# Performance work log

Measured on AMD Instinct MI355X. Metric: run time of the kernel, lower is better.

Reference implementation:

```python
import jax, jax.numpy as jnp
import numpy as np
from jax import lax

EPS = 1e-5
NUM_GROUPS = 32
OFFSET_SCALE = 1.0
K = 3            # deformable conv kernel size
KK = K * K
DWK = 7          # depthwise kernel size for offset predictor


def group_norm(x, gamma, beta, num_groups=NUM_GROUPS):
    B, C, H, W = x.shape
    xg = x.reshape(B, num_groups, C // num_groups, H, W)
    m = xg.mean(axis=(2, 3, 4), keepdims=True)
    v = xg.var(axis=(2, 3, 4), keepdims=True)
    xn = ((xg - m) * lax.rsqrt(v + EPS)).reshape(B, C, H, W)
    return xn * gamma[None, :, None, None] + beta[None, :, None, None]


def bilinear_gather(x, py, px):
    # x: [B,C,H,W]; py, px: [B,KK,H,W] absolute sample coords -> [B,C,KK,H,W]
    B, C, H, W = x.shape
    y0 = jnp.floor(py)
    x0 = jnp.floor(px)
    wy1 = py - y0
    wx1 = px - x0
    wy0 = 1.0 - wy1
    wx0 = 1.0 - wx1
    xf = x.reshape(B, C, H * W)

    def gather(yi, xi):
        valid = (yi >= 0) & (yi <= H - 1) & (xi >= 0) & (xi <= W - 1)
        yc = jnp.clip(yi, 0, H - 1).astype(jnp.int32)
        xc = jnp.clip(xi, 0, W - 1).astype(jnp.int32)
        idx = (yc * W + xc).reshape(B, -1)                      # [B, KK*H*W]
        g = jax.vmap(lambda a, i: a[:, i])(xf, idx)             # [B, C, KK*H*W]
        g = g.reshape(B, C, KK, H, W)
        return g * valid.astype(x.dtype)[:, None]

    out = (gather(y0, x0) * (wy0 * wx0)[:, None]
           + gather(y0, x0 + 1.0) * (wy0 * wx1)[:, None]
           + gather(y0 + 1.0, x0) * (wy1 * wx0)[:, None]
           + gather(y0 + 1.0, x0 + 1.0) * (wy1 * wx1)[:, None])
    return out


def deform_conv(x, dw, pw, pwb, w, b):
    # x: [B,C,H,W]; dw: [C,1,DWK,DWK] depthwise; pw: [2*KK,C,1,1]; w: [O,C,K,K]
    B, C, H, W = x.shape
    dn = ('NCHW', 'OIHW', 'NCHW')
    f = lax.conv_general_dilated(x, dw, (1, 1), 'SAME',
                                 feature_group_count=C, dimension_numbers=dn)
    off = lax.conv_general_dilated(f, pw, (1, 1), 'SAME', dimension_numbers=dn)
    off = (off + pwb[None, :, None, None]) * OFFSET_SCALE       # [B,2*KK,H,W]
    off = off.reshape(B, KK, 2, H, W)
    ks = jnp.arange(K, dtype=x.dtype) - (K - 1) / 2             # [-1,0,1]
    ky = jnp.repeat(ks, K)                                      # [KK]
    kx = jnp.tile(ks, K)
    yy, xx = jnp.meshgrid(jnp.arange(H, dtype=x.dtype),
                          jnp.arange(W, dtype=x.dtype), indexing='ij')
    py = yy[None, None] + ky[None, :, None, None] + off[:, :, 0]  # [B,KK,H,W]
    px = xx[None, None] + kx[None, :, None, None] + off[:, :, 1]
    sampled = bilinear_gather(x, py, px)                        # [B,C,KK,H,W]
    O = w.shape[0]
    out = jnp.einsum('bckhw,ock->bohw', sampled, w.reshape(O, C, KK))
    return out + b[None, :, None, None]


def setup_inputs() -> dict:
    key = jax.random.key(0)
    ks = jax.random.split(key, 10)
    B, C, H, W = 4, 256, 64, 64
    O = C
    x = jax.random.normal(ks[0], (B, C, H, W), dtype=jnp.float32)

    def conv_w(k, shape, fan_in):
        return jax.random.normal(k, shape, dtype=jnp.float32) / np.sqrt(fan_in)

    inp = {
        'x': x,
        'gn1_g': jnp.ones((C,), jnp.float32), 'gn1_b': jnp.zeros((C,), jnp.float32),
        'dw1': conv_w(ks[1], (C, 1, DWK, DWK), DWK * DWK),
        'pw1': jax.random.normal(ks[2], (2 * KK, C, 1, 1), jnp.float32) * 0.01,
        'pwb1': jnp.zeros((2 * KK,), jnp.float32),
        'w1': conv_w(ks[3], (O, C, K, K), C * KK),
        'b1': jnp.zeros((O,), jnp.float32),
        'gn2_g': jnp.ones((O,), jnp.float32), 'gn2_b': jnp.zeros((O,), jnp.float32),
        'dw2': conv_w(ks[4], (O, 1, DWK, DWK), DWK * DWK),
        'pw2': jax.random.normal(ks[5], (2 * KK, O, 1, 1), jnp.float32) * 0.01,
        'pwb2': jnp.zeros((2 * KK,), jnp.float32),
        'w2': conv_w(ks[6], (O, O, K, K), O * KK),
        'b2': jnp.zeros((O,), jnp.float32),
    }
    return inp


def reference(x, gn1_g, gn1_b, dw1, pw1, pwb1, w1, b1,
              gn2_g, gn2_b, dw2, pw2, pwb2, w2, b2):
    h = jax.nn.relu(group_norm(x, gn1_g, gn1_b))
    h = deform_conv(h, dw1, pw1, pwb1, w1, b1)
    h = jax.nn.relu(group_norm(h, gn2_g, gn2_b))
    # Dropout / DropPath are identity in eval mode
    h = deform_conv(h, dw2, pw2, pwb2, w2, b2)
    return h + x  # shortcut is Identity (in_channels == out_channels)
```

## Files before the change

kernel.cpp:

```cpp
#include <hip/hip_runtime.h>

#define B_    4
#define C_    256
#define H_    64
#define W_    64
#define HW_   4096
#define NG_   32
#define CPG_  8
#define KK_   9
#define NOFF_ 18

typedef __attribute__((ext_vector_type(8))) short short8;
typedef __attribute__((ext_vector_type(4))) short short4v;
typedef __attribute__((ext_vector_type(4))) float floatx4;

static __device__ __forceinline__ short f2bf(float f) {
    union { float f; unsigned u; } v; v.f = f;
    unsigned r = v.u + 0x7fff + ((v.u >> 16) & 1);
    return (short)(r >> 16);
}
static __device__ __forceinline__ float bf2f(short s) {
    union { unsigned u; float f; } v;
    v.u = ((unsigned)(unsigned short)s) << 16;
    return v.f;
}

__global__ __launch_bounds__(256) void prep_kernel(
    const float* __restrict__ w1, const float* __restrict__ w2,
    const float* __restrict__ pw1, const float* __restrict__ pw2,
    const float* __restrict__ x,
    short* __restrict__ wp1, short* __restrict__ wp2,
    short* __restrict__ ppk1, short* __restrict__ ppk2,
    float2* __restrict__ stats1, float* __restrict__ gsum,
    float* __restrict__ gss)
{
    int blk = blockIdx.x;
    int t = threadIdx.x;
    if (blk < 4608) {
        const float* w = (blk < 2304) ? w1 : w2;
        short* wp = (blk < 2304) ? wp1 : wp2;
        int idx = (blk % 2304) * 256 + t;
        int j    = idx & 7;
        int lane = (idx >> 3) & 63;
        int ot   = (idx >> 9) & 15;
        int slab = idx >> 13;
        int k = slab >> 3, cc = slab & 7;
        int o = ot * 16 + (lane & 15);
        int c = cc * 32 + (lane >> 4) * 8 + j;
        wp[idx] = f2bf(w[(size_t)(o * C_ + c) * KK_ + k]);
    } else if (blk < 4672) {
        int q = blk - 4608;
        const float* pw = (q < 32) ? pw1 : pw2;
        short* ppk = (q < 32) ? ppk1 : ppk2;
        int idx = (q & 31) * 256 + t;
        int j = idx & 7, lane = (idx >> 3) & 63;
        int ot = (idx >> 9) & 1, sl = idx >> 10;
        int o = ot * 16 + (lane & 15);
        int k = sl * 32 + (lane >> 4) * 8 + j;
        ppk[idx] = (o < NOFF_) ? f2bf(pw[o * C_ + k]) : (short)0;
    } else if (blk < 4800) {
        int q = blk - 4672;
        size_t base = (size_t)q * CPG_ * HW_;
        const float4* in4 = (const float4*)(x + base);
        float s = 0.f, ss = 0.f;
        for (int i = t; i < 8192; i += 256) {
            float4 v = in4[i];
            s  += v.x + v.y + v.z + v.w;
            ss += v.x * v.x + v.y * v.y + v.z * v.z + v.w * v.w;
        }
        #pragma unroll
        for (int d = 32; d > 0; d >>= 1) {
            s  += __shfl_down(s, d, 64);
            ss += __shfl_down(ss, d, 64);
        }
        __shared__ float red[8];
        int wid = t >> 6;
        if ((t & 63) == 0) { red[wid] = s; red[4 + wid] = ss; }
        __syncthreads();
        if (t == 0) {
            float S  = red[0] + red[1] + red[2] + red[3];
            float SS = red[4] + red[5] + red[6] + red[7];
            float m = S / 32768.f;
            float var = SS / 32768.f - m * m;
            stats1[q] = make_float2(m, rsqrtf(var + 1e-5f));
        }
    } else {
        if (t < 128) { gsum[t] = 0.f; gss[t] = 0.f; }
    }
}

__global__ __launch_bounds__(256) void gnt_kernel(
    const float* __restrict__ xin, const short* __restrict__ yin,
    const float2* __restrict__ stats1, const float* __restrict__ gsum,
    const float* __restrict__ gss, const float* __restrict__ gamma,
    const float* __restrict__ beta, short* __restrict__ hbf,
    short* __restrict__ hbt, int layer)
{
    int q = blockIdx.x;
    int b = q >> 6;
    int px0 = (q & 63) * 64;
    __shared__ unsigned ltile[64 * 132];
    __shared__ float2 sst[32];
    int t = threadIdx.x;
    if (t < 32) {
        float m, rs;
        if (layer == 1) { float2 v = stats1[b * 32 + t]; m = v.x; rs = v.y; }
        else {
            float s = gsum[b * 32 + t], ss = gss[b * 32 + t];
            m = s / 32768.f;
            float var = ss / 32768.f - m * m;
            rs = rsqrtf(var + 1e-5f);
        }
        sst[t] = make_float2(m, rs);
    }
    __syncthreads();
    int pq4 = t & 15, cphi = t >> 4;
    #pragma unroll
    for (int i = 0; i < 8; ++i) {
        int cp = i * 16 + cphi;
        int c0 = 2 * cp, c1 = c0 + 1;
        float2 st = sst[c0 >> 3];
        float ga0 = gamma[c0] * st.y, be0 = beta[c0] - st.x * ga0;
        float ga1 = gamma[c1] * st.y, be1 = beta[c1] - st.x * ga1;
        short4v lo, hi;
        if (layer == 1) {
            const float* r0 = xin + (size_t)(b * C_ + c0) * HW_ + px0 + pq4 * 4;
            float4 v0 = *(const float4*)r0;
            float4 v1 = *(const float4*)(r0 + HW_);
            lo.x = f2bf(fmaxf(fmaf(v0.x, ga0, be0), 0.f));
            lo.y = f2bf(fmaxf(fmaf(v0.y, ga0, be0), 0.f));
            lo.z = f2bf(fmaxf(fmaf(v0.z, ga0, be0), 0.f));
            lo.w = f2bf(fmaxf(fmaf(v0.w, ga0, be0), 0.f));
            hi.x = f2bf(fmaxf(fmaf(v1.x, ga1, be1), 0.f));
            hi.y = f2bf(fmaxf(fmaf(v1.y, ga1, be1), 0.f));
            hi.z = f2bf(fmaxf(fmaf(v1.z, ga1, be1), 0.f));
            hi.w = f2bf(fmaxf(fmaf(v1.w, ga1, be1), 0.f));
        } else {
            const short* r0 = yin + (size_t)(b * C_ + c0) * HW_ + px0 + pq4 * 4;
            short4v v0 = *(const short4v*)r0;
            short4v v1 = *(const short4v*)(r0 + HW_);
            lo.x = f2bf(fmaxf(fmaf(bf2f(v0.x), ga0, be0), 0.f));
            lo.y = f2bf(fmaxf(fmaf(bf2f(v0.y), ga0, be0), 0.f));
            lo.z = f2bf(fmaxf(fmaf(bf2f(v0.z), ga0, be0), 0.f));
            lo.w = f2bf(fmaxf(fmaf(bf2f(v0.w), ga0, be0), 0.f));
            hi.x = f2bf(fmaxf(fmaf(bf2f(v1.x), ga1, be1), 0.f));
            hi.y = f2bf(fmaxf(fmaf(bf2f(v1.y), ga1, be1), 0.f));
            hi.z = f2bf(fmaxf(fmaf(bf2f(v1.z), ga1, be1), 0.f));
            hi.w = f2bf(fmaxf(fmaf(bf2f(v1.w), ga1, be1), 0.f));
        }
        *(short4v*)(hbf + (size_t)(b * C_ + c0) * HW_ + px0 + pq4 * 4) = lo;
        *(short4v*)(hbf + (size_t)(b * C_ + c1) * HW_ + px0 + pq4 * 4) = hi;
        #pragma unroll
        for (int j = 0; j < 4; ++j) {
            int pl = pq4 * 4 + j;
            unsigned wrd = (unsigned)(unsigned short)lo[j]
                         | ((unsigned)(unsigned short)hi[j] << 16);
            ltile[pl * 132 + (cp ^ ((pl & 7) << 2))] = wrd;
        }
    }
    __syncthreads();
    int co = t & 31, ph = t >> 5;
    #pragma unroll
    for (int r = 0; r < 8; ++r) {
        int pl = r * 8 + ph;
        uint4 v = *(const uint4*)&ltile[pl * 132 + ((co * 4) ^ ((pl & 7) << 2))];
        *(uint4*)(hbt + ((size_t)b * HW_ + px0 + pl) * C_ + co * 8) = v;
    }
}

__global__ __launch_bounds__(256) void dw7_kernel(
    const short* __restrict__ in, const float* __restrict__ dwk,
    short* __restrict__ out)
{
    int plane = blockIdx.x;
    int c = plane & (C_ - 1);
    const short* src = in + (size_t)plane * HW_;
    short* dst = out + (size_t)plane * HW_;
    __shared__ float tile[70 * 72];
    __shared__ float wk[49];
    int t = threadIdx.x;
    if (t < 49) wk[t] = dwk[c * 49 + t];
    for (int i = t; i < 70 * 72; i += 256) tile[i] = 0.f;
    __syncthreads();
    const short4v* src4 = (const short4v*)src;
    for (int i = t; i < HW_ / 4; i += 256) {
        short4v v = src4[i];
        int y = i >> 4, x = (i & 15) * 4;
        float* tp = &tile[(y + 3) * 72 + (x + 3)];
        tp[0] = bf2f(v.x); tp[1] = bf2f(v.y);
        tp[2] = bf2f(v.z); tp[3] = bf2f(v.w);
    }
    __syncthreads();
    #pragma unroll
    for (int it = 0; it < 4; ++it) {
        int idx = it * 256 + t;
        int y = idx >> 4;
        int x0 = (idx & 15) * 4;
        float a0 = 0.f, a1 = 0.f, a2 = 0.f, a3 = 0.f;
        #pragma unroll
        for (int dy = 0; dy < 7; ++dy) {
            const float* tr = &tile[(y + dy) * 72 + x0];
            float4 ra = *(const float4*)tr;
            float4 rb = *(const float4*)(tr + 4);
            float4 rc = *(const float4*)(tr + 8);
            float r[12] = {ra.x, ra.y, ra.z, ra.w,
                           rb.x, rb.y, rb.z, rb.w,
                           rc.x, rc.y, rc.z, rc.w};
            const float* wr = &wk[dy * 7];
            #pragma unroll
            for (int dx = 0; dx < 7; ++dx) {
                float wv = wr[dx];
                a0 = fmaf(r[dx], wv, a0);
                a1 = fmaf(r[dx + 1], wv, a1);
                a2 = fmaf(r[dx + 2], wv, a2);
                a3 = fmaf(r[dx + 3], wv, a3);
            }
        }
        short4v o;
        o.x = f2bf(a0); o.y = f2bf(a1); o.z = f2bf(a2); o.w = f2bf(a3);
        *(short4v*)&dst[y * 64 + x0] = o;
    }
}

__global__ __launch_bounds__(1024, 4) void deform_fused_kernel(
    const short* __restrict__ hbt,  const short* __restrict__ fdwc,
    const short* __restrict__ ppk,  const float* __restrict__ pwb,
    const short* __restrict__ wp,   const float* __restrict__ bias,
    const float* __restrict__ resid, float* __restrict__ outf,
    short* __restrict__ outb, float* __restrict__ gsum,
    float* __restrict__ gss)
{
    int b = blockIdx.x >> 6;
    int row = blockIdx.x & 63;
    __shared__ __align__(16) short sbuf[2][16384];
    __shared__ int   pidx[576];
    __shared__ float cf[576][4];
    __shared__ float off_lds[NOFF_ * 64];
    int t = threadIdx.x;
    int wv = t >> 6, lane = t & 63;
    int pq = lane >> 4, pr = lane & 15;

    short* ftile = &sbuf[0][0];
    {
        int c = t >> 2, seg = t & 3;
        const short* src = fdwc + (size_t)(b * C_ + c) * HW_ + row * 64;
        *(short8*)&ftile[c * 64 + seg * 8]       = *(const short8*)(src + seg * 8);
        *(short8*)&ftile[c * 64 + (seg + 4) * 8] = *(const short8*)(src + (seg + 4) * 8);
    }
    __syncthreads();

    if (wv < 8) {
        int ot = wv & 1, ptw = wv >> 1;
        int pxl = ptw * 16 + pr;
        const short8* ap = (const short8*)ppk;
        floatx4 pacc = (floatx4){0.f, 0.f, 0.f, 0.f};
        #pragma unroll
        for (int sl = 0; sl < 8; ++sl) {
            short8 bf;
            int cbase = sl * 32 + pq * 8;
            #pragma unroll
            for (int j = 0; j < 8; ++j) bf[j] = ftile[(cbase + j) * 64 + pxl];
            short8 af = ap[(sl * 2 + ot) * 64 + lane];
            pacc = __builtin_amdgcn_mfma_f32_16x16x32_bf16(af, bf, pacc, 0, 0, 0);
        }
        #pragma unroll
        for (int r = 0; r < 4; ++r) {
            int o = ot * 16 + pq * 4 + r;
            if (o < NOFF_) off_lds[o * 64 + pxl] = pacc[r] + pwb[o];
        }
    }
    __syncthreads();

    if (t < 576) {
        int k = t >> 6, p = t & 63;
        float offy = off_lds[(2 * k) * 64 + p];
        float offx = off_lds[(2 * k + 1) * 64 + p];
        float py = (float)row + (float)(k / 3 - 1) + offy;
        float px = (float)p   + (float)(k % 3 - 1) + offx;
        float y0f = floorf(py), x0f = floorf(px);
        float wy1 = py - y0f, wx1 = px - x0f;
        float wy0 = 1.f - wy1, wx0 = 1.f - wx1;
        float y1f = y0f + 1.f, x1f = x0f + 1.f;
        bool vy0 = (y0f >= 0.f) && (y0f <= 63.f);
        bool vy1 = (y1f >= 0.f) && (y1f <= 63.f);
        bool vx0 = (x0f >= 0.f) && (x0f <= 63.f);
        bool vx1 = (x1f >= 0.f) && (x1f <= 63.f);
        int iy0 = (int)fminf(fmaxf(y0f, 0.f), 63.f);
        int iy1 = (int)fminf(fmaxf(y1f, 0.f), 63.f);
        int ix0 = (int)fminf(fmaxf(x0f, 0.f), 63.f);
        int ix1 = (int)fminf(fmaxf(x1f, 0.f), 63.f);
        pidx[t] = iy0 | (ix0 << 8) | (iy1 << 16) | (ix1 << 24);
        cf[t][0] = (vy0 && vx0) ? wy0 * wx0 : 0.f;
        cf[t][1] = (vy0 && vx1) ? wy0 * wx1 : 0.f;
        cf[t][2] = (vy1 && vx0) ? wy1 * wx0 : 0.f;
        cf[t][3] = (vy1 && vx1) ? wy1 * wx1 : 0.f;
    }
    __syncthreads();

    int ssl0 = t >> 8;
    int spx = (t >> 2) & 63, scb = t & 3;
    int u2 = spx * 4 + (scb ^ ((spx + (spx >> 2)) & 3));
    const short* hb0 = hbt + ((size_t)b * HW_) * C_ + ssl0 * 32 + scb * 8;
    const short* hb1 = hb0 + 128;

    short8 rs0[8], rs1[8];
    auto prefetch = [&](int g, short8* r) {
        int pk = pidx[g * 64 + spx];
        int iy0 = pk & 255, ix0 = (pk >> 8) & 255;
        int iy1 = (pk >> 16) & 255, ix1 = (pk >> 24) & 255;
        size_t a00 = (size_t)(iy0 * 64 + ix0) * C_;
        size_t a01 = (size_t)(iy0 * 64 + ix1) * C_;
        size_t a10 = (size_t)(iy1 * 64 + ix0) * C_;
        size_t a11 = (size_t)(iy1 * 64 + ix1) * C_;
        r[0] = *(const short8*)(hb0 + a00);
        r[1] = *(const short8*)(hb0 + a01);
        r[2] = *(const short8*)(hb0 + a10);
        r[3] = *(const short8*)(hb0 + a11);
        r[4] = *(const short8*)(hb1 + a00);
        r[5] = *(const short8*)(hb1 + a01);
        r[6] = *(const short8*)(hb1 + a10);
        r[7] = *(const short8*)(hb1 + a11);
    };
    auto stage_write = [&](int g, int bi, const short8* r) {
        int e = g * 64 + spx;
        float w00 = cf[e][0], w01 = cf[e][1], w10 = cf[e][2], w11 = cf[e][3];
        short8 va, vb;
        #pragma unroll
        for (int j = 0; j < 8; ++j) {
            va[j] = f2bf(w00 * bf2f(r[0][j]) + w01 * bf2f(r[1][j])
                       + w10 * bf2f(r[2][j]) + w11 * bf2f(r[3][j]));
            vb[j] = f2bf(w00 * bf2f(r[4][j]) + w01 * bf2f(r[5][j])
                       + w10 * bf2f(r[6][j]) + w11 * bf2f(r[7][j]));
        }
        *(short8*)&sbuf[bi][ssl0 * 2048 + u2 * 8] = va;
        *(short8*)&sbuf[bi][(ssl0 + 4) * 2048 + u2 * 8] = vb;
    };

    floatx4 acc[4];
    #pragma unroll
    for (int pt = 0; pt < 4; ++pt) acc[pt] = (floatx4){0.f, 0.f, 0.f, 0.f};
    int ub[4];
    #pragma unroll
    for (int pt = 0; pt < 4; ++pt) {
        int px2 = pt * 16 + pr;
        ub[pt] = px2 * 4 + (pq ^ ((px2 + (px2 >> 2)) & 3));
    }

    prefetch(0, rs0);
    stage_write(0, 0, rs0);
    prefetch(1, rs1);
    __syncthreads();

    const short8* wp8 = (const short8*)wp;
    #pragma unroll
    for (int g = 0; g < 9; ++g) {
        if (g + 2 < 9) prefetch(g + 2, (g & 1) ? rs1 : rs0);
        const short* sb = sbuf[g & 1];
        #pragma unroll
        for (int half = 0; half < 2; ++half) {
            short8 af[4];
            #pragma unroll
            for (int q2 = 0; q2 < 4; ++q2)
                af[q2] = wp8[(size_t)((g * 8 + half * 4 + q2) * 16 + wv) * 64 + lane];
            #pragma unroll
            for (int q2 = 0; q2 < 4; ++q2) {
                int s2 = half * 4 + q2;
                #pragma unroll
                for (int pt = 0; pt < 4; ++pt) {
                    short8 bfv = *(const short8*)&sb[s2 * 2048 + ub[pt] * 8];
                    acc[pt] = __builtin_amdgcn_mfma_f32_16x16x32_bf16(
                        af[q2], bfv, acc[pt], 0, 0, 0);
                }
            }
        }
        if (g + 1 < 9)
            stage_write(g + 1, (g + 1) & 1, (g & 1) ? rs0 : rs1);
        __syncthreads();
    }

    float ssum = 0.f, ssq = 0.f;
    #pragma unroll
    for (int r = 0; r < 4; ++r) {
        int o = wv * 16 + pq * 4 + r;
        float bo = bias[o];
        size_t obase = ((size_t)(b * C_ + o)) * HW_ + row * 64 + pr;
        #pragma unroll
        for (int pt = 0; pt < 4; ++pt) {
            float v = acc[pt][r] + bo;
            if (outf) {
                outf[obase + pt * 16] = v + resid[obase + pt * 16];
            } else {
                short sv = f2bf(v);
                outb[obase + pt * 16] = sv;
                float vq = bf2f(sv);
                ssum += vq; ssq += vq * vq;
            }
        }
    }
    if (outb) {
        #pragma unroll
        for (int d = 1; d < 32; d <<= 1) {
            ssum += __shfl_xor(ssum, d, 64);
            ssq  += __shfl_xor(ssq, d, 64);
        }
        if ((lane & 31) == 0) {
            int grp = wv * 2 + (pq >> 1);
            atomicAdd(&gsum[b * 32 + grp], ssum);
            atomicAdd(&gss[b * 32 + grp], ssq);
        }
    }
}

extern "C" void kernel_launch(void* const* d_in, const int* in_sizes, int n_in,
                              void* d_out, int out_size, void* d_ws, size_t ws_size,
                              hipStream_t stream)
{
    const float* x     = (const float*)d_in[0];
    const float* gn1_g = (const float*)d_in[1];
    const float* gn1_b = (const float*)d_in[2];
    const float* dw1   = (const float*)d_in[3];
    const float* pw1   = (const float*)d_in[4];
    const float* pwb1  = (const float*)d_in[5];
    const float* w1    = (const float*)d_in[6];
    const float* b1    = (const float*)d_in[7];
    const float* gn2_g = (const float*)d_in[8];
    const float* gn2_b = (const float*)d_in[9];
    const float* dw2   = (const float*)d_in[10];
    const float* pw2   = (const float*)d_in[11];
    const float* pwb2  = (const float*)d_in[12];
    const float* w2    = (const float*)d_in[13];
    const float* b2    = (const float*)d_in[14];
    float* out = (float*)d_out;

    float* ws   = (float*)d_ws;
    short* y1b    = (short*)ws;
    short* hbf    = (short*)(ws + 2097152);
    short* hbt    = (short*)(ws + 4194304);
    short* fdwc   = (short*)(ws + 6291456);
    short* wp1    = (short*)(ws + 8388608);
    short* wp2    = (short*)(ws + 8683520);
    short* ppk1   = (short*)(ws + 8978432);
    short* ppk2   = (short*)(ws + 8982528);
    float2* st1   = (float2*)(ws + 8986624);
    float* gsum   = ws + 8986880;
    float* gss    = ws + 8987008;

    prep_kernel<<<4801, 256, 0, stream>>>(w1, w2, pw1, pw2, x,
                                          wp1, wp2, ppk1, ppk2,
                                          st1, gsum, gss);

    gnt_kernel<<<256, 256, 0, stream>>>(x, nullptr, st1, gsum, gss,
                                        gn1_g, gn1_b, hbf, hbt, 1);
    dw7_kernel<<<B_ * C_, 256, 0, stream>>>(hbf, dw1, fdwc);
    deform_fused_kernel<<<B_ * H_, 1024, 0, stream>>>(
        hbt, fdwc, ppk1, pwb1, wp1, b1, nullptr, nullptr, y1b, gsum, gss);

    gnt_kernel<<<256, 256, 0, stream>>>(nullptr, y1b, st1, gsum, gss,
                                        gn2_g, gn2_b, hbf, hbt, 2);
    dw7_kernel<<<B_ * C_, 256, 0, stream>>>(hbf, dw2, fdwc);
    deform_fused_kernel<<<B_ * H_, 1024, 0, stream>>>(
        hbt, fdwc, ppk2, pwb2, wp2, b2, x, out, nullptr, nullptr, nullptr);
}
```

Baseline: 263.6 us.

## Fuse all stages into one cooperative persistent kernel with grid syncs

```diff
diff --git a/kernel.cpp b/kernel.cpp
--- a/kernel.cpp
+++ b/kernel.cpp
@@ -1,4 +1,7 @@
 #include <hip/hip_runtime.h>
+#include <hip/hip_cooperative_groups.h>
+
+namespace cg = cooperative_groups;
 
 #define B_    4
 #define C_    256
@@ -25,99 +28,31 @@
     return v.f;
 }
 
-__global__ __launch_bounds__(256) void prep_kernel(
-    const float* __restrict__ w1, const float* __restrict__ w2,
-    const float* __restrict__ pw1, const float* __restrict__ pw2,
-    const float* __restrict__ x,
-    short* __restrict__ wp1, short* __restrict__ wp2,
-    short* __restrict__ ppk1, short* __restrict__ ppk2,
-    float2* __restrict__ stats1, float* __restrict__ gsum,
-    float* __restrict__ gss)
+static __device__ __forceinline__ void gnt_phase(
+    char* smem, int layer, const float* xin, const short* yin,
+    const float2* st1, const float* gsum, const float* gss,
+    const float* gamma, const float* beta, short* hbt)
 {
-    int blk = blockIdx.x;
-    int t = threadIdx.x;
-    if (blk < 4608) {
-        const float* w = (blk < 2304) ? w1 : w2;
-        short* wp = (blk < 2304) ? wp1 : wp2;
-        int idx = (blk % 2304) * 256 + t;
-        int j    = idx & 7;
-        int lane = (idx >> 3) & 63;
-        int ot   = (idx >> 9) & 15;
-        int slab = idx >> 13;
-        int k = slab >> 3, cc = slab & 7;
-        int o = ot * 16 + (lane & 15);
-        int c = cc * 32 + (lane >> 4) * 8 + j;
-        wp[idx] = f2bf(w[(size_t)(o * C_ + c) * KK_ + k]);
-    } else if (blk < 4672) {
-        int q = blk - 4608;
-        const float* pw = (q < 32) ? pw1 : pw2;
-        short* ppk = (q < 32) ? ppk1 : ppk2;
-        int idx = (q & 31) * 256 + t;
-        int j = idx & 7, lane = (idx >> 3) & 63;
-        int ot = (idx >> 9) & 1, sl = idx >> 10;
-        int o = ot * 16 + (lane & 15);
-        int k = sl * 32 + (lane >> 4) * 8 + j;
-        ppk[idx] = (o < NOFF_) ? f2bf(pw[o * C_ + k]) : (short)0;
-    } else if (blk < 4800) {
-        int q = blk - 4672;
-        size_t base = (size_t)q * CPG_ * HW_;
-        const float4* in4 = (const float4*)(x + base);
-        float s = 0.f, ss = 0.f;
-        for (int i = t; i < 8192; i += 256) {
-            float4 v = in4[i];
-            s  += v.x + v.y + v.z + v.w;
-            ss += v.x * v.x + v.y * v.y + v.z * v.z + v.w * v.w;
-        }
-        #pragma unroll
-        for (int d = 32; d > 0; d >>= 1) {
-            s  += __shfl_down(s, d, 64);
-            ss += __shfl_down(ss, d, 64);
-        }
-        __shared__ float red[8];
-        int wid = t >> 6;
-        if ((t & 63) == 0) { red[wid] = s; red[4 + wid] = ss; }
-        __syncthreads();
-        if (t == 0) {
-            float S  = red[0] + red[1] + red[2] + red[3];
-            float SS = red[4] + red[5] + red[6] + red[7];
-            float m = S / 32768.f;
-            float var = SS / 32768.f - m * m;
-            stats1[q] = make_float2(m, rsqrtf(var + 1e-5f));
-        }
-    } else {
-        if (t < 128) { gsum[t] = 0.f; gss[t] = 0.f; }
-    }
-}
-
-__global__ __launch_bounds__(256) void gnt_kernel(
-    const float* __restrict__ xin, const short* __restrict__ yin,
-    const float2* __restrict__ stats1, const float* __restrict__ gsum,
-    const float* __restrict__ gss, const float* __restrict__ gamma,
-    const float* __restrict__ beta, short* __restrict__ hbf,
-    short* __restrict__ hbt, int layer)
-{
-    int q = blockIdx.x;
-    int b = q >> 6;
-    int px0 = (q & 63) * 64;
-    __shared__ unsigned ltile[64 * 132];
-    __shared__ float2 sst[32];
-    int t = threadIdx.x;
+    unsigned* ltile = (unsigned*)smem;
+    float2* sst = (float2*)(smem + 33792);
+    int blk = blockIdx.x, t = threadIdx.x;
+    int b = blk >> 6;
+    int px0 = (blk & 63) * 64;
     if (t < 32) {
         float m, rs;
-        if (layer == 1) { float2 v = stats1[b * 32 + t]; m = v.x; rs = v.y; }
+        if (layer == 1) { float2 v = st1[b * 32 + t]; m = v.x; rs = v.y; }
         else {
             float s = gsum[b * 32 + t], ss = gss[b * 32 + t];
             m = s / 32768.f;
-            float var = ss / 32768.f - m * m;
-            rs = rsqrtf(var + 1e-5f);
+            rs = rsqrtf(ss / 32768.f - m * m + 1e-5f);
         }
         sst[t] = make_float2(m, rs);
     }
     __syncthreads();
     int pq4 = t & 15, cphi = t >> 4;
     #pragma unroll
-    for (int i = 0; i < 8; ++i) {
-        int cp = i * 16 + cphi;
+    for (int i = 0; i < 2; ++i) {
+        int cp = i * 64 + cphi;
         int c0 = 2 * cp, c1 = c0 + 1;
         float2 st = sst[c0 >> 3];
         float ga0 = gamma[c0] * st.y, be0 = beta[c0] - st.x * ga0;
@@ -148,8 +83,6 @@
             hi.z = f2bf(fmaxf(fmaf(bf2f(v1.z), ga1, be1), 0.f));
             hi.w = f2bf(fmaxf(fmaf(bf2f(v1.w), ga1, be1), 0.f));
         }
-        *(short4v*)(hbf + (size_t)(b * C_ + c0) * HW_ + px0 + pq4 * 4) = lo;
-        *(short4v*)(hbf + (size_t)(b * C_ + c1) * HW_ + px0 + pq4 * 4) = hi;
         #pragma unroll
         for (int j = 0; j < 4; ++j) {
             int pl = pq4 * 4 + j;
@@ -161,39 +94,64 @@
     __syncthreads();
     int co = t & 31, ph = t >> 5;
     #pragma unroll
-    for (int r = 0; r < 8; ++r) {
-        int pl = r * 8 + ph;
+    for (int r = 0; r < 2; ++r) {
+        int pl = r * 32 + ph;
         uint4 v = *(const uint4*)&ltile[pl * 132 + ((co * 4) ^ ((pl & 7) << 2))];
         *(uint4*)(hbt + ((size_t)b * HW_ + px0 + pl) * C_ + co * 8) = v;
     }
 }
 
-__global__ __launch_bounds__(256) void dw7_kernel(
-    const short* __restrict__ in, const float* __restrict__ dwk,
-    short* __restrict__ out)
+static __device__ __forceinline__ void dw7_phase(
+    char* smem, int layer, const float* xin, const short* yin,
+    const float2* st1, const float* gsum, const float* gss,
+    const float* gamma, const float* beta, const float* dwk,
+    short* fdwc)
 {
-    int plane = blockIdx.x;
-    int c = plane & (C_ - 1);
-    const short* src = in + (size_t)plane * HW_;
-    short* dst = out + (size_t)plane * HW_;
-    __shared__ float tile[70 * 72];
-    __shared__ float wk[49];
     int t = threadIdx.x;
-    if (t < 49) wk[t] = dwk[c * 49 + t];
-    for (int i = t; i < 70 * 72; i += 256) tile[i] = 0.f;
-    __syncthreads();
-    const short4v* src4 = (const short4v*)src;
-    for (int i = t; i < HW_ / 4; i += 256) {
-        short4v v = src4[i];
-        int y = i >> 4, x = (i & 15) * 4;
-        float* tp = &tile[(y + 3) * 72 + (x + 3)];
-        tp[0] = bf2f(v.x); tp[1] = bf2f(v.y);
-        tp[2] = bf2f(v.z); tp[3] = bf2f(v.w);
-    }
-    __syncthreads();
+    int q = t >> 8, tq = t & 255;
+    int plane = blockIdx.x * 4 + q;
+    int b = plane >> 8, c = plane & (C_ - 1);
+    float* tile = (float*)(smem + q * 20480);
+    float* wk = tile + 5040;
+    float m, rs;
+    if (layer == 1) { float2 s = st1[b * 32 + (c >> 3)]; m = s.x; rs = s.y; }
+    else {
+        float s = gsum[b * 32 + (c >> 3)], ss = gss[b * 32 + (c >> 3)];
+        m = s / 32768.f;
+        rs = rsqrtf(ss / 32768.f - m * m + 1e-5f);
+    }
+    float ga = gamma[c] * rs, be = beta[c] - m * ga;
+    if (tq < 49) wk[tq] = dwk[c * 49 + tq];
+    for (int i = tq; i < 5040; i += 256) tile[i] = 0.f;
+    __syncthreads();
+    if (layer == 1) {
+        const float4* src4 = (const float4*)(xin + (size_t)plane * HW_);
+        for (int i = tq; i < 1024; i += 256) {
+            float4 v = src4[i];
+            int y = i >> 4, xx = (i & 15) * 4;
+            float* tp = &tile[(y + 3) * 72 + xx + 3];
+            tp[0] = fmaxf(fmaf(v.x, ga, be), 0.f);
+            tp[1] = fmaxf(fmaf(v.y, ga, be), 0.f);
+            tp[2] = fmaxf(fmaf(v.z, ga, be), 0.f);
+            tp[3] = fmaxf(fmaf(v.w, ga, be), 0.f);
+        }
+    } else {
+        const short4v* src4 = (const short4v*)(yin + (size_t)plane * HW_);
+        for (int i = tq; i < 1024; i += 256) {
+            short4v v = src4[i];
+            int y = i >> 4, xx = (i & 15) * 4;
+            float* tp = &tile[(y + 3) * 72 + xx + 3];
+            tp[0] = fmaxf(fmaf(bf2f(v.x), ga, be), 0.f);
+            tp[1] = fmaxf(fmaf(bf2f(v.y), ga, be), 0.f);
+            tp[2] = fmaxf(fmaf(bf2f(v.z), ga, be), 0.f);
+            tp[3] = fmaxf(fmaf(bf2f(v.w), ga, be), 0.f);
+        }
+    }
+    __syncthreads();
+    short* dst = fdwc + (size_t)plane * HW_;
     #pragma unroll
     for (int it = 0; it < 4; ++it) {
-        int idx = it * 256 + t;
+        int idx = it * 256 + tq;
         int y = idx >> 4;
         int x0 = (idx & 15) * 4;
         float a0 = 0.f, a1 = 0.f, a2 = 0.f, a3 = 0.f;
@@ -222,30 +180,28 @@
     }
 }
 
-__global__ __launch_bounds__(1024, 4) void deform_fused_kernel(
-    const short* __restrict__ hbt,  const short* __restrict__ fdwc,
-    const short* __restrict__ ppk,  const float* __restrict__ pwb,
-    const short* __restrict__ wp,   const float* __restrict__ bias,
-    const float* __restrict__ resid, float* __restrict__ outf,
-    short* __restrict__ outb, float* __restrict__ gsum,
-    float* __restrict__ gss)
+static __device__ __forceinline__ void deform_phase(
+    char* smem, const short* hbt, const short* fdwc, const short* ppk,
+    const float* pwb, const short* wp, const float* bias,
+    const float* resid, float* outf, short* outb,
+    float* gsum, float* gss)
 {
+    short* sbufA = (short*)smem;
+    short* sbufB = (short*)(smem + 32768);
+    int*   pidx  = (int*)(smem + 65536);
+    float (*cf)[4] = (float(*)[4])(smem + 67840);
+    float* off_lds = (float*)(smem + 77056);
     int b = blockIdx.x >> 6;
     int row = blockIdx.x & 63;
-    __shared__ __align__(16) short sbuf[2][16384];
-    __shared__ int   pidx[576];
-    __shared__ float cf[576][4];
-    __shared__ float off_lds[NOFF_ * 64];
     int t = threadIdx.x;
     int wv = t >> 6, lane = t & 63;
     int pq = lane >> 4, pr = lane & 15;
 
-    short* ftile = &sbuf[0][0];
     {
         int c = t >> 2, seg = t & 3;
         const short* src = fdwc + (size_t)(b * C_ + c) * HW_ + row * 64;
-        *(short8*)&ftile[c * 64 + seg * 8]       = *(const short8*)(src + seg * 8);
-        *(short8*)&ftile[c * 64 + (seg + 4) * 8] = *(const short8*)(src + (seg + 4) * 8);
+        *(short8*)&sbufA[c * 64 + seg * 8]       = *(const short8*)(src + seg * 8);
+        *(short8*)&sbufA[c * 64 + (seg + 4) * 8] = *(const short8*)(src + (seg + 4) * 8);
     }
     __syncthreads();
 
@@ -259,7 +215,7 @@
             short8 bf;
             int cbase = sl * 32 + pq * 8;
             #pragma unroll
-            for (int j = 0; j < 8; ++j) bf[j] = ftile[(cbase + j) * 64 + pxl];
+            for (int j = 0; j < 8; ++j) bf[j] = sbufA[(cbase + j) * 64 + pxl];
             short8 af = ap[(sl * 2 + ot) * 64 + lane];
             pacc = __builtin_amdgcn_mfma_f32_16x16x32_bf16(af, bf, pacc, 0, 0, 0);
         }
@@ -332,8 +288,9 @@
             vb[j] = f2bf(w00 * bf2f(r[4][j]) + w01 * bf2f(r[5][j])
                        + w10 * bf2f(r[6][j]) + w11 * bf2f(r[7][j]));
         }
-        *(short8*)&sbuf[bi][ssl0 * 2048 + u2 * 8] = va;
-        *(short8*)&sbuf[bi][(ssl0 + 4) * 2048 + u2 * 8] = vb;
+        short* sb = bi ? sbufB : sbufA;
+        *(short8*)&sb[ssl0 * 2048 + u2 * 8] = va;
+        *(short8*)&sb[(ssl0 + 4) * 2048 + u2 * 8] = vb;
     };
 
     floatx4 acc[4];
@@ -352,10 +309,8 @@
     __syncthreads();
 
     const short8* wp8 = (const short8*)wp;
-    #pragma unroll
     for (int g = 0; g < 9; ++g) {
-        if (g + 2 < 9) prefetch(g + 2, (g & 1) ? rs1 : rs0);
-        const short* sb = sbuf[g & 1];
+        const short* sb = (g & 1) ? sbufB : sbufA;
         #pragma unroll
         for (int half = 0; half < 2; ++half) {
             short8 af[4];
@@ -373,8 +328,10 @@
                 }
             }
         }
-        if (g + 1 < 9)
+        if (g + 1 < 9) {
             stage_write(g + 1, (g + 1) & 1, (g & 1) ? rs0 : rs1);
+            if (g + 2 < 9) prefetch(g + 2, (g & 1) ? rs1 : rs0);
+        }
         __syncthreads();
     }
 
@@ -409,6 +366,106 @@
             atomicAdd(&gss[b * 32 + grp], ssq);
         }
     }
+}
+
+__global__ __launch_bounds__(1024) void mono_kernel(
+    const float* __restrict__ x,
+    const float* __restrict__ gn1_g, const float* __restrict__ gn1_b,
+    const float* __restrict__ dw1, const float* __restrict__ pw1,
+    const float* __restrict__ pwb1, const float* __restrict__ w1,
+    const float* __restrict__ b1,
+    const float* __restrict__ gn2_g, const float* __restrict__ gn2_b,
+    const float* __restrict__ dw2, const float* __restrict__ pw2,
+    const float* __restrict__ pwb2, const float* __restrict__ w2,
+    const float* __restrict__ b2,
+    float* __restrict__ out,
+    short* __restrict__ hbt1, short* __restrict__ fdwc1,
+    short* __restrict__ hbt2, short* __restrict__ fdwc2,
+    short* __restrict__ y1b,
+    short* __restrict__ wp1, short* __restrict__ wp2,
+    short* __restrict__ ppk1, short* __restrict__ ppk2,
+    float2* __restrict__ st1, float* __restrict__ gsum,
+    float* __restrict__ gss)
+{
+    cg::grid_group grid = cg::this_grid();
+    __shared__ __align__(16) char smem[81920];
+    int blk = blockIdx.x, t = threadIdx.x;
+
+    if (blk < 128) {
+        size_t base = (size_t)blk * CPG_ * HW_;
+        const float4* in4 = (const float4*)(x + base);
+        float s = 0.f, ss = 0.f;
+        for (int i = t; i < 8192; i += 1024) {
+            float4 v = in4[i];
+            s  += v.x + v.y + v.z + v.w;
+            ss += v.x * v.x + v.y * v.y + v.z * v.z + v.w * v.w;
+        }
+        #pragma unroll
+        for (int d = 32; d > 0; d >>= 1) {
+            s  += __shfl_down(s, d, 64);
+            ss += __shfl_down(ss, d, 64);
+        }
+        float* red = (float*)smem;
+        int wid = t >> 6;
+        if ((t & 63) == 0) { red[wid] = s; red[16 + wid] = ss; }
+        __syncthreads();
+        if (t == 0) {
+            float S = 0.f, SS = 0.f;
+            #pragma unroll
+            for (int i = 0; i < 16; ++i) { S += red[i]; SS += red[16 + i]; }
+            float m = S / 32768.f;
+            float var = SS / 32768.f - m * m;
+            st1[blk] = make_float2(m, rsqrtf(var + 1e-5f));
+        }
+    } else {
+        int tid = (blk - 128) * 1024 + t;
+        for (int idx = tid; idx < 589824; idx += 131072) {
+            int j    = idx & 7;
+            int lane = (idx >> 3) & 63;
+            int ot   = (idx >> 9) & 15;
+            int slab = idx >> 13;
+            int k = slab >> 3, cc = slab & 7;
+            int o = ot * 16 + (lane & 15);
+            int c = cc * 32 + (lane >> 4) * 8 + j;
+            wp1[idx] = f2bf(w1[(size_t)(o * C_ + c) * KK_ + k]);
+            wp2[idx] = f2bf(w2[(size_t)(o * C_ + c) * KK_ + k]);
+        }
+        if (tid < 8192) {
+            int j = tid & 7, lane = (tid >> 3) & 63;
+            int ot = (tid >> 9) & 1, sl = tid >> 10;
+            int o = ot * 16 + (lane & 15);
+            int k = sl * 32 + (lane >> 4) * 8 + j;
+            ppk1[tid] = (o < NOFF_) ? f2bf(pw1[o * C_ + k]) : (short)0;
+            ppk2[tid] = (o < NOFF_) ? f2bf(pw2[o * C_ + k]) : (short)0;
+        }
+        if (blk == 128 && t < 128) { gsum[t] = 0.f; gss[t] = 0.f; }
+    }
+    __threadfence();
+    grid.sync();
+    __threadfence();
+
+    gnt_phase(smem, 1, x, nullptr, st1, gsum, gss, gn1_g, gn1_b, hbt1);
+    __syncthreads();
+    dw7_phase(smem, 1, x, nullptr, st1, gsum, gss, gn1_g, gn1_b, dw1, fdwc1);
+    __threadfence();
+    grid.sync();
+    __threadfence();
+
+    deform_phase(smem, hbt1, fdwc1, ppk1, pwb1, wp1, b1,
+                 nullptr, nullptr, y1b, gsum, gss);
+    __threadfence();
+    grid.sync();
+    __threadfence();
+
+    gnt_phase(smem, 2, nullptr, y1b, st1, gsum, gss, gn2_g, gn2_b, hbt2);
+    __syncthreads();
+    dw7_phase(smem, 2, nullptr, y1b, st1, gsum, gss, gn2_g, gn2_b, dw2, fdwc2);
+    __threadfence();
+    grid.sync();
+    __threadfence();
+
+    deform_phase(smem, hbt2, fdwc2, ppk2, pwb2, wp2, b2,
+                 x, out, nullptr, nullptr, nullptr);
 }
 
 extern "C" void kernel_launch(void* const* d_in, const int* in_sizes, int n_in,
@@ -432,32 +489,29 @@
     const float* b2    = (const float*)d_in[14];
     float* out = (float*)d_out;
 
-    float* ws   = (float*)d_ws;
-    short* y1b    = (short*)ws;
-    short* hbf    = (short*)(ws + 2097152);
-    short* hbt    = (short*)(ws + 4194304);
-    short* fdwc   = (short*)(ws + 6291456);
-    short* wp1    = (short*)(ws + 8388608);
-    short* wp2    = (short*)(ws + 8683520);
-    short* ppk1   = (short*)(ws + 8978432);
-    short* ppk2   = (short*)(ws + 8982528);
-    float2* st1   = (float2*)(ws + 8986624);
-    float* gsum   = ws + 8986880;
-    float* gss    = ws + 8987008;
-
-    prep_kernel<<<4801, 256, 0, stream>>>(w1, w2, pw1, pw2, x,
-                                          wp1, wp2, ppk1, ppk2,
-                                          st1, gsum, gss);
-
-    gnt_kernel<<<256, 256, 0, stream>>>(x, nullptr, st1, gsum, gss,
-                                        gn1_g, gn1_b, hbf, hbt, 1);
-    dw7_kernel<<<B_ * C_, 256, 0, stream>>>(hbf, dw1, fdwc);
-    deform_fused_kernel<<<B_ * H_, 1024, 0, stream>>>(
-        hbt, fdwc, ppk1, pwb1, wp1, b1, nullptr, nullptr, y1b, gsum, gss);
-
-    gnt_kernel<<<256, 256, 0, stream>>>(nullptr, y1b, st1, gsum, gss,
-                                        gn2_g, gn2_b, hbf, hbt, 2);
-    dw7_kernel<<<B_ * C_, 256, 0, stream>>>(hbf, dw2, fdwc);
-    deform_fused_kernel<<<B_ * H_, 1024, 0, stream>>>(
-        hbt, fdwc, ppk2, pwb2, wp2, b2, x, out, nullptr, nullptr, nullptr);
-}
+    float* ws = (float*)d_ws;
+    short* hbt1  = (short*)ws;
+    short* fdwc1 = (short*)(ws + 2097152);
+    short* hbt2  = (short*)(ws + 4194304);
+    short* fdwc2 = (short*)(ws + 6291456);
+    short* y1b   = (short*)(ws + 8388608);
+    short* wp1   = (short*)(ws + 10485760);
+    short* wp2   = (short*)(ws + 10780672);
+    short* ppk1  = (short*)(ws + 11075584);
+    short* ppk2  = (short*)(ws + 11079680);
+    float2* st1  = (float2*)(ws + 11083776);
+    float* gsum  = ws + 11084032;
+    float* gss   = ws + 11084160;
+
+    void* args[] = {
+        (void*)&x, (void*)&gn1_g, (void*)&gn1_b, (void*)&dw1, (void*)&pw1,
+        (void*)&pwb1, (void*)&w1, (void*)&b1, (void*)&gn2_g, (void*)&gn2_b,
+        (void*)&dw2, (void*)&pw2, (void*)&pwb2, (void*)&w2, (void*)&b2,
+        (void*)&out,
+        (void*)&hbt1, (void*)&fdwc1, (void*)&hbt2, (void*)&fdwc2, (void*)&y1b,
+        (void*)&wp1, (void*)&wp2, (void*)&ppk1, (void*)&ppk2,
+        (void*)&st1, (void*)&gsum, (void*)&gss
+    };
+    hipLaunchCooperativeKernel((void*)mono_kernel, dim3(256), dim3(1024),
+                               args, 0, stream);
+}
```

New measurement: 1.037 ms. 293% more time.

## Fuse GroupNorm transpose and depthwise 7x7 into one dual-role kernel launch

Applied to the files above, without the earlier changes.

```diff
diff --git a/kernel.cpp b/kernel.cpp
--- a/kernel.cpp
+++ b/kernel.cpp
@@ -89,136 +89,154 @@
     }
 }
 
-__global__ __launch_bounds__(256) void gnt_kernel(
-    const float* __restrict__ xin, const short* __restrict__ yin,
-    const float2* __restrict__ stats1, const float* __restrict__ gsum,
+__global__ __launch_bounds__(1024) void gd_kernel(
+    int layer, const float* __restrict__ xin, const short* __restrict__ yin,
+    const float2* __restrict__ st1, const float* __restrict__ gsum,
     const float* __restrict__ gss, const float* __restrict__ gamma,
-    const float* __restrict__ beta, short* __restrict__ hbf,
-    short* __restrict__ hbt, int layer)
+    const float* __restrict__ beta, const float* __restrict__ dwk,
+    short* __restrict__ hbt, short* __restrict__ fdwc)
 {
-    int q = blockIdx.x;
-    int b = q >> 6;
-    int px0 = (q & 63) * 64;
-    __shared__ unsigned ltile[64 * 132];
-    __shared__ float2 sst[32];
+    __shared__ __align__(16) char smem[81920];
     int t = threadIdx.x;
-    if (t < 32) {
+    if (blockIdx.x < 256) {
+        int blk = blockIdx.x;
+        unsigned* ltile = (unsigned*)smem;
+        float2* sst = (float2*)(smem + 33792);
+        int b = blk >> 6;
+        int px0 = (blk & 63) * 64;
+        if (t < 32) {
+            float m, rs;
+            if (layer == 1) { float2 v = st1[b * 32 + t]; m = v.x; rs = v.y; }
+            else {
+                float s = gsum[b * 32 + t], ss = gss[b * 32 + t];
+                m = s / 32768.f;
+                rs = rsqrtf(ss / 32768.f - m * m + 1e-5f);
+            }
+            sst[t] = make_float2(m, rs);
+        }
+        __syncthreads();
+        int pq4 = t & 15, cphi = t >> 4;
+        #pragma unroll
+        for (int i = 0; i < 2; ++i) {
+            int cp = i * 64 + cphi;
+            int c0 = 2 * cp, c1 = c0 + 1;
+            float2 st = sst[c0 >> 3];
+            float ga0 = gamma[c0] * st.y, be0 = beta[c0] - st.x * ga0;
+            float ga1 = gamma[c1] * st.y, be1 = beta[c1] - st.x * ga1;
+            short4v lo, hi;
+            if (layer == 1) {
+                const float* r0 = xin + (size_t)(b * C_ + c0) * HW_ + px0 + pq4 * 4;
+                float4 v0 = *(const float4*)r0;
+                float4 v1 = *(const float4*)(r0 + HW_);
+                lo.x = f2bf(fmaxf(fmaf(v0.x, ga0, be0), 0.f));
+                lo.y = f2bf(fmaxf(fmaf(v0.y, ga0, be0), 0.f));
+                lo.z = f2bf(fmaxf(fmaf(v0.z, ga0, be0), 0.f));
+                lo.w = f2bf(fmaxf(fmaf(v0.w, ga0, be0), 0.f));
+                hi.x = f2bf(fmaxf(fmaf(v1.x, ga1, be1), 0.f));
+                hi.y = f2bf(fmaxf(fmaf(v1.y, ga1, be1), 0.f));
+                hi.z = f2bf(fmaxf(fmaf(v1.z, ga1, be1), 0.f));
+                hi.w = f2bf(fmaxf(fmaf(v1.w, ga1, be1), 0.f));
+            } else {
+                const short* r0 = yin + (size_t)(b * C_ + c0) * HW_ + px0 + pq4 * 4;
+                short4v v0 = *(const short4v*)r0;
+                short4v v1 = *(const short4v*)(r0 + HW_);
+                lo.x = f2bf(fmaxf(fmaf(bf2f(v0.x), ga0, be0), 0.f));
+                lo.y = f2bf(fmaxf(fmaf(bf2f(v0.y), ga0, be0), 0.f));
+                lo.z = f2bf(fmaxf(fmaf(bf2f(v0.z), ga0, be0), 0.f));
+                lo.w = f2bf(fmaxf(fmaf(bf2f(v0.w), ga0, be0), 0.f));
+                hi.x = f2bf(fmaxf(fmaf(bf2f(v1.x), ga1, be1), 0.f));
+                hi.y = f2bf(fmaxf(fmaf(bf2f(v1.y), ga1, be1), 0.f));
+                hi.z = f2bf(fmaxf(fmaf(bf2f(v1.z), ga1, be1), 0.f));
+                hi.w = f2bf(fmaxf(fmaf(bf2f(v1.w), ga1, be1), 0.f));
+            }
+            #pragma unroll
+            for (int j = 0; j < 4; ++j) {
+                int pl = pq4 * 4 + j;
+                unsigned wrd = (unsigned)(unsigned short)lo[j]
+                             | ((unsigned)(unsigned short)hi[j] << 16);
+                ltile[pl * 132 + (cp ^ ((pl & 7) << 2))] = wrd;
+            }
+        }
+        __syncthreads();
+        int co = t & 31, ph = t >> 5;
+        #pragma unroll
+        for (int r = 0; r < 2; ++r) {
+            int pl = r * 32 + ph;
+            uint4 v = *(const uint4*)&ltile[pl * 132 + ((co * 4) ^ ((pl & 7) << 2))];
+            *(uint4*)(hbt + ((size_t)b * HW_ + px0 + pl) * C_ + co * 8) = v;
+        }
+    } else {
+        int blk = blockIdx.x - 256;
+        int q = t >> 8, tq = t & 255;
+        int plane = blk * 4 + q;
+        int b = plane >> 8, c = plane & (C_ - 1);
+        float* tile = (float*)(smem + q * 20480);
+        float* wk = tile + 5040;
         float m, rs;
-        if (layer == 1) { float2 v = stats1[b * 32 + t]; m = v.x; rs = v.y; }
+        if (layer == 1) { float2 s = st1[b * 32 + (c >> 3)]; m = s.x; rs = s.y; }
         else {
-            float s = gsum[b * 32 + t], ss = gss[b * 32 + t];
+            float s = gsum[b * 32 + (c >> 3)], ss = gss[b * 32 + (c >> 3)];
             m = s / 32768.f;
-            float var = ss / 32768.f - m * m;
-            rs = rsqrtf(var + 1e-5f);
-        }
-        sst[t] = make_float2(m, rs);
-    }
-    __syncthreads();
-    int pq4 = t & 15, cphi = t >> 4;
-    #pragma unroll
-    for (int i = 0; i < 8; ++i) {
-        int cp = i * 16 + cphi;
-        int c0 = 2 * cp, c1 = c0 + 1;
-        float2 st = sst[c0 >> 3];
-        float ga0 = gamma[c0] * st.y, be0 = beta[c0] - st.x * ga0;
-        float ga1 = gamma[c1] * st.y, be1 = beta[c1] - st.x * ga1;
-        short4v lo, hi;
+            rs = rsqrtf(ss / 32768.f - m * m + 1e-5f);
+        }
+        float ga = gamma[c] * rs, be = beta[c] - m * ga;
+        if (tq < 49) wk[tq] = dwk[c * 49 + tq];
+        for (int i = tq; i < 5040; i += 256) tile[i] = 0.f;
+        __syncthreads();
         if (layer == 1) {
-            const float* r0 = xin + (size_t)(b * C_ + c0) * HW_ + px0 + pq4 * 4;
-            float4 v0 = *(const float4*)r0;
-            float4 v1 = *(const float4*)(r0 + HW_);
-            lo.x = f2bf(fmaxf(fmaf(v0.x, ga0, be0), 0.f));
-            lo.y = f2bf(fmaxf(fmaf(v0.y, ga0, be0), 0.f));
-            lo.z = f2bf(fmaxf(fmaf(v0.z, ga0, be0), 0.f));
-            lo.w = f2bf(fmaxf(fmaf(v0.w, ga0, be0), 0.f));
-            hi.x = f2bf(fmaxf(fmaf(v1.x, ga1, be1), 0.f));
-            hi.y = f2bf(fmaxf(fmaf(v1.y, ga1, be1), 0.f));
-            hi.z = f2bf(fmaxf(fmaf(v1.z, ga1, be1), 0.f));
-            hi.w = f2bf(fmaxf(fmaf(v1.w, ga1, be1), 0.f));
+            const float4* src4 = (const float4*)(xin + (size_t)plane * HW_);
+            for (int i = tq; i < 1024; i += 256) {
+                float4 v = src4[i];
+                int y = i >> 4, xx = (i & 15) * 4;
+                float* tp = &tile[(y + 3) * 72 + xx + 3];
+                tp[0] = fmaxf(fmaf(v.x, ga, be), 0.f);
+                tp[1] = fmaxf(fmaf(v.y, ga, be), 0.f);
+                tp[2] = fmaxf(fmaf(v.z, ga, be), 0.f);
+                tp[3] = fmaxf(fmaf(v.w, ga, be), 0.f);
+            }
         } else {
-            const short* r0 = yin + (size_t)(b * C_ + c0) * HW_ + px0 + pq4 * 4;
-            short4v v0 = *(const short4v*)r0;
-            short4v v1 = *(const short4v*)(r0 + HW_);
-            lo.x = f2bf(fmaxf(fmaf(bf2f(v0.x), ga0, be0), 0.f));
-            lo.y = f2bf(fmaxf(fmaf(bf2f(v0.y), ga0, be0), 0.f));
-            lo.z = f2bf(fmaxf(fmaf(bf2f(v0.z), ga0, be0), 0.f));
-            lo.w = f2bf(fmaxf(fmaf(bf2f(v0.w), ga0, be0), 0.f));
-            hi.x = f2bf(fmaxf(fmaf(bf2f(v1.x), ga1, be1), 0.f));
-            hi.y = f2bf(fmaxf(fmaf(bf2f(v1.y), ga1, be1), 0.f));
-            hi.z = f2bf(fmaxf(fmaf(bf2f(v1.z), ga1, be1), 0.f));
-            hi.w = f2bf(fmaxf(fmaf(bf2f(v1.w), ga1, be1), 0.f));
-        }
-        *(short4v*)(hbf + (size_t)(b * C_ + c0) * HW_ + px0 + pq4 * 4) = lo;
-        *(short4v*)(hbf + (size_t)(b * C_ + c1) * HW_ + px0 + pq4 * 4) = hi;
-        #pragma unroll
-        for (int j = 0; j < 4; ++j) {
-            int pl = pq4 * 4 + j;
-            unsigned wrd = (unsigned)(unsigned short)lo[j]
-                         | ((unsigned)(unsigned short)hi[j] << 16);
-            ltile[pl * 132 + (cp ^ ((pl & 7) << 2))] = wrd;
-        }
-    }
-    __syncthreads();
-    int co = t & 31, ph = t >> 5;
-    #pragma unroll
-    for (int r = 0; r < 8; ++r) {
-        int pl = r * 8 + ph;
-        uint4 v = *(const uint4*)&ltile[pl * 132 + ((co * 4) ^ ((pl & 7) << 2))];
-        *(uint4*)(hbt + ((size_t)b * HW_ + px0 + pl) * C_ + co * 8) = v;
-    }
-}
-
-__global__ __launch_bounds__(256) void dw7_kernel(
-    const short* __restrict__ in, const float* __restrict__ dwk,
-    short* __restrict__ out)
-{
-    int plane = blockIdx.x;
-    int c = plane & (C_ - 1);
-    const short* src = in + (size_t)plane * HW_;
-    short* dst = out + (size_t)plane * HW_;
-    __shared__ float tile[70 * 72];
-    __shared__ float wk[49];
-    int t = threadIdx.x;
-    if (t < 49) wk[t] = dwk[c * 49 + t];
-    for (int i = t; i < 70 * 72; i += 256) tile[i] = 0.f;
-    __syncthreads();
-    const short4v* src4 = (const short4v*)src;
-    for (int i = t; i < HW_ / 4; i += 256) {
-        short4v v = src4[i];
-        int y = i >> 4, x = (i & 15) * 4;
-        float* tp = &tile[(y + 3) * 72 + (x + 3)];
-        tp[0] = bf2f(v.x); tp[1] = bf2f(v.y);
-        tp[2] = bf2f(v.z); tp[3] = bf2f(v.w);
-    }
-    __syncthreads();
-    #pragma unroll
-    for (int it = 0; it < 4; ++it) {
-        int idx = it * 256 + t;
-        int y = idx >> 4;
-        int x0 = (idx & 15) * 4;
-        float a0 = 0.f, a1 = 0.f, a2 = 0.f, a3 = 0.f;
-        #pragma unroll
-        for (int dy = 0; dy < 7; ++dy) {
-            const float* tr = &tile[(y + dy) * 72 + x0];
-            float4 ra = *(const float4*)tr;
-            float4 rb = *(const float4*)(tr + 4);
-            float4 rc = *(const float4*)(tr + 8);
-            float r[12] = {ra.x, ra.y, ra.z, ra.w,
-                           rb.x, rb.y, rb.z, rb.w,
-                           rc.x, rc.y, rc.z, rc.w};
-            const float* wr = &wk[dy * 7];
+            const short4v* src4 = (const short4v*)(yin + (size_t)plane * HW_);
+            for (int i = tq; i < 1024; i += 256) {
+                short4v v = src4[i];
+                int y = i >> 4, xx = (i & 15) * 4;
+                float* tp = &tile[(y + 3) * 72 + xx + 3];
+                tp[0] = fmaxf(fmaf(bf2f(v.x), ga, be), 0.f);
+                tp[1] = fmaxf(fmaf(bf2f(v.y), ga, be), 0.f);
+                tp[2] = fmaxf(fmaf(bf2f(v.z), ga, be), 0.f);
+                tp[3] = fmaxf(fmaf(bf2f(v.w), ga, be), 0.f);
+            }
+        }
+        __syncthreads();
+        short* dst = fdwc + (size_t)plane * HW_;
+        #pragma unroll
+        for (int it = 0; it < 4; ++it) {
+            int idx = it * 256 + tq;
+            int y = idx >> 4;
+            int x0 = (idx & 15) * 4;
+            float a0 = 0.f, a1 = 0.f, a2 = 0.f, a3 = 0.f;
             #pragma unroll
-            for (int dx = 0; dx < 7; ++dx) {
-                float wv = wr[dx];
-                a0 = fmaf(r[dx], wv, a0);
-                a1 = fmaf(r[dx + 1], wv, a1);
-                a2 = fmaf(r[dx + 2], wv, a2);
-                a3 = fmaf(r[dx + 3], wv, a3);
-            }
-        }
-        short4v o;
-        o.x = f2bf(a0); o.y = f2bf(a1); o.z = f2bf(a2); o.w = f2bf(a3);
-        *(short4v*)&dst[y * 64 + x0] = o;
+            for (int dy = 0; dy < 7; ++dy) {
+                const float* tr = &tile[(y + dy) * 72 + x0];
+                float4 ra = *(const float4*)tr;
+                float4 rb = *(const float4*)(tr + 4);
+                float4 rc = *(const float4*)(tr + 8);
+                float r[12] = {ra.x, ra.y, ra.z, ra.w,
+                               rb.x, rb.y, rb.z, rb.w,
+                               rc.x, rc.y, rc.z, rc.w};
+                const float* wr = &wk[dy * 7];
+                #pragma unroll
+                for (int dx = 0; dx < 7; ++dx) {
+                    float wv = wr[dx];
+                    a0 = fmaf(r[dx], wv, a0);
+                    a1 = fmaf(r[dx + 1], wv, a1);
+                    a2 = fmaf(r[dx + 2], wv, a2);
+                    a3 = fmaf(r[dx + 3], wv, a3);
+                }
+            }
+            short4v o;
+            o.x = f2bf(a0); o.y = f2bf(a1); o.z = f2bf(a2); o.w = f2bf(a3);
+            *(short4v*)&dst[y * 64 + x0] = o;
+        }
     }
 }
 
@@ -240,12 +258,11 @@
     int wv = t >> 6, lane = t & 63;
     int pq = lane >> 4, pr = lane & 15;
 
-    short* ftile = &sbuf[0][0];
     {
         int c = t >> 2, seg = t & 3;
         const short* src = fdwc + (size_t)(b * C_ + c) * HW_ + row * 64;
-        *(short8*)&ftile[c * 64 + seg * 8]       = *(const short8*)(src + seg * 8);
-        *(short8*)&ftile[c * 64 + (seg + 4) * 8] = *(const short8*)(src + (seg + 4) * 8);
+        *(short8*)&sbuf[0][c * 64 + seg * 8]       = *(const short8*)(src + seg * 8);
+        *(short8*)&sbuf[0][c * 64 + (seg + 4) * 8] = *(const short8*)(src + (seg + 4) * 8);
     }
     __syncthreads();
 
@@ -259,7 +276,7 @@
             short8 bf;
             int cbase = sl * 32 + pq * 8;
             #pragma unroll
-            for (int j = 0; j < 8; ++j) bf[j] = ftile[(cbase + j) * 64 + pxl];
+            for (int j = 0; j < 8; ++j) bf[j] = sbuf[0][(cbase + j) * 64 + pxl];
             short8 af = ap[(sl * 2 + ot) * 64 + lane];
             pacc = __builtin_amdgcn_mfma_f32_16x16x32_bf16(af, bf, pacc, 0, 0, 0);
         }
@@ -332,8 +349,9 @@
             vb[j] = f2bf(w00 * bf2f(r[4][j]) + w01 * bf2f(r[5][j])
                        + w10 * bf2f(r[6][j]) + w11 * bf2f(r[7][j]));
         }
-        *(short8*)&sbuf[bi][ssl0 * 2048 + u2 * 8] = va;
-        *(short8*)&sbuf[bi][(ssl0 + 4) * 2048 + u2 * 8] = vb;
+        short* sb = sbuf[bi];
+        *(short8*)&sb[ssl0 * 2048 + u2 * 8] = va;
+        *(short8*)&sb[(ssl0 + 4) * 2048 + u2 * 8] = vb;
     };
 
     floatx4 acc[4];
@@ -432,32 +450,29 @@
     const float* b2    = (const float*)d_in[14];
     float* out = (float*)d_out;
 
-    float* ws   = (float*)d_ws;
-    short* y1b    = (short*)ws;
-    short* hbf    = (short*)(ws + 2097152);
-    short* hbt    = (short*)(ws + 4194304);
-    short* fdwc   = (short*)(ws + 6291456);
-    short* wp1    = (short*)(ws + 8388608);
-    short* wp2    = (short*)(ws + 8683520);
-    short* ppk1   = (short*)(ws + 8978432);
-    short* ppk2   = (short*)(ws + 8982528);
-    float2* st1   = (float2*)(ws + 8986624);
-    float* gsum   = ws + 8986880;
-    float* gss    = ws + 8987008;
+    float* ws = (float*)d_ws;
+    short* y1b   = (short*)ws;
+    short* hbt   = (short*)(ws + 2097152);
+    short* fdwc  = (short*)(ws + 4194304);
+    short* wp1   = (short*)(ws + 6291456);
+    short* wp2   = (short*)(ws + 6586368);
+    short* ppk1  = (short*)(ws + 6881280);
+    short* ppk2  = (short*)(ws + 6885376);
+    float2* st1  = (float2*)(ws + 6889472);
+    float* gsum  = ws + 6889728;
+    float* gss   = ws + 6889856;
 
     prep_kernel<<<4801, 256, 0, stream>>>(w1, w2, pw1, pw2, x,
                                           wp1, wp2, ppk1, ppk2,
                                           st1, gsum, gss);
 
-    gnt_kernel<<<256, 256, 0, stream>>>(x, nullptr, st1, gsum, gss,
-                                        gn1_g, gn1_b, hbf, hbt, 1);
-    dw7_kernel<<<B_ * C_, 256, 0, stream>>>(hbf, dw1, fdwc);
+    gd_kernel<<<512, 1024, 0, stream>>>(1, x, nullptr, st1, gsum, gss,
+                                        gn1_g, gn1_b, dw1, hbt, fdwc);
     deform_fused_kernel<<<B_ * H_, 1024, 0, stream>>>(
         hbt, fdwc, ppk1, pwb1, wp1, b1, nullptr, nullptr, y1b, gsum, gss);
 
-    gnt_kernel<<<256, 256, 0, stream>>>(nullptr, y1b, st1, gsum, gss,
-                                        gn2_g, gn2_b, hbf, hbt, 2);
-    dw7_kernel<<<B_ * C_, 256, 0, stream>>>(hbf, dw2, fdwc);
+    gd_kernel<<<512, 1024, 0, stream>>>(2, nullptr, y1b, st1, gsum, gss,
+                                        gn2_g, gn2_b, dw2, hbt, fdwc);
     deform_fused_kernel<<<B_ * H_, 1024, 0, stream>>>(
         hbt, fdwc, ppk2, pwb2, wp2, b2, x, out, nullptr, nullptr, nullptr);
 }
```

After: 258.9 us. Within noise of the previous version (-1.8%).
